# Optimization experiments

Measured on AMD Instinct MI355X. Metric: run time of the kernel, lower is better.

## Reference

```python
import jax, jax.numpy as jnp
import numpy as np

N_SKILLS = 1000
N_PROBLEMS = 20000
EMB = 256
TIME_LOG = 5.0
B, S = 32, 2048


def setup_inputs() -> dict:
    key = jax.random.key(0)
    ks = jax.random.split(key, 10)
    skills = jax.random.randint(ks[0], (B, S), 0, N_SKILLS, dtype=jnp.int64) if jax.config.jax_enable_x64 else jax.random.randint(ks[0], (B, S), 0, N_SKILLS, dtype=jnp.int32)
    problems = jax.random.randint(ks[1], (B, S), 0, N_PROBLEMS, dtype=skills.dtype)
    times = jnp.sort(jax.random.randint(ks[2], (B, S), 0, 10_000_000, dtype=skills.dtype), axis=-1)
    labels = jax.random.randint(ks[3], (B, S), 0, 2, dtype=skills.dtype)
    std = 0.01
    alpha_inter_W = std * jax.random.normal(ks[4], (2 * N_SKILLS, EMB), dtype=jnp.float32)
    alpha_skill_W = std * jax.random.normal(ks[5], (N_SKILLS, EMB), dtype=jnp.float32)
    beta_inter_W = std * jax.random.normal(ks[6], (2 * N_SKILLS, EMB), dtype=jnp.float32)
    beta_skill_W = std * jax.random.normal(ks[7], (N_SKILLS, EMB), dtype=jnp.float32)
    problem_base_W = std * jax.random.normal(ks[8], (N_PROBLEMS, 1), dtype=jnp.float32)
    skill_base_W = std * jax.random.normal(ks[9], (N_SKILLS, 1), dtype=jnp.float32)
    return {
        "skills": skills, "problems": problems, "times": times, "labels": labels,
        "alpha_inter_W": alpha_inter_W, "alpha_skill_W": alpha_skill_W,
        "beta_inter_W": beta_inter_W, "beta_skill_W": beta_skill_W,
        "problem_base_W": problem_base_W, "skill_base_W": skill_base_W,
    }


def reference(skills, problems, times, labels,
              alpha_inter_W, alpha_skill_W, beta_inter_W, beta_skill_W,
              problem_base_W, skill_base_W):
    n_skills = alpha_skill_W.shape[0]
    inters = skills + labels * n_skills  # [B,S]

    alpha_src = alpha_inter_W[inters]      # [B,S,E]
    alpha_tgt = alpha_skill_W[skills]      # [B,S,E]
    alphas = jnp.einsum("bse,bte->bst", alpha_src, alpha_tgt)  # [B,S,S]

    beta_src = beta_inter_W[inters]
    beta_tgt = beta_skill_W[skills]
    betas = jnp.einsum("bse,bte->bst", beta_src, beta_tgt)
    betas = jnp.clip(betas + 1.0, 0.0, 10.0)

    t = times.astype(jnp.float32) / 1000.0
    delta_t = jnp.abs(t[:, :, None] - t[:, None, :])
    delta_t = jnp.log(delta_t + 1e-10) / jnp.log(jnp.float32(TIME_LOG))

    cross = alphas * jnp.exp(-betas * delta_t)  # [B,S,S]

    seq_len = skills.shape[1]
    # original keeps strict upper triangle (source i strictly before target j)
    keep = jnp.triu(jnp.ones((seq_len, seq_len), dtype=cross.dtype), k=1)
    sum_t = jnp.sum(cross * keep[None], axis=-2)  # sum over source dim -> [B,S]

    problem_bias = problem_base_W[problems][..., 0]  # [B,S]
    skill_bias = skill_base_W[skills][..., 0]        # [B,S]
    h = problem_bias + skill_bias + sum_t
    return jax.nn.sigmoid(h)
```

## Files before the change

### kernel.cpp

```cpp
#include <hip/hip_runtime.h>
#include <hip/hip_bf16.h>
#include <stdint.h>

#define NSK   1000
#define EMB   256
#define BB    32
#define SS    2048
#define TILE  128
#define NJT   (SS / TILE)
#define NUNIT (NJT * (NJT + 1) / 2)
#define BK    32
#define NCHUNK (EMB / BK)
#define SCALE_INV (1.0f / 4096.0f)

typedef float f32x16 __attribute__((ext_vector_type(16)));
typedef float f32x4  __attribute__((ext_vector_type(4)));
typedef long  longx2 __attribute__((ext_vector_type(2)));

#define OFF_AI8 0
#define OFF_BI8 (2 * NSK * EMB)
#define OFF_AS8 (4 * NSK * EMB)
#define OFF_BS8 (5 * NSK * EMB)
#define TOT8    (6 * NSK * EMB)

__global__ void cvt_tables(const float* __restrict__ ai, const float* __restrict__ bi,
                           const float* __restrict__ as_, const float* __restrict__ bs,
                           int* __restrict__ ws8, float* __restrict__ acc) {
    int g = blockIdx.x * 256 + threadIdx.x;
    if (g < BB * SS) acc[g] = 0.0f;
    if (g * 4 >= TOT8) return;
    int e = g * 4;
    const float* src; int off;
    if (e < OFF_AS8) { if (e < OFF_BI8) { src = ai;  off = e; }
                       else             { src = bi;  off = e - OFF_BI8; } }
    else             { if (e < OFF_BS8) { src = as_; off = e - OFF_AS8; }
                       else             { src = bs;  off = e - OFF_BS8; } }
    const float4 v = *(const float4*)(src + off);
    int lo = __builtin_amdgcn_cvt_pk_fp8_f32(v.x * 64.0f, v.y * 64.0f, 0, false);
    int wd = __builtin_amdgcn_cvt_pk_fp8_f32(v.z * 64.0f, v.w * 64.0f, lo, true);
    ws8[g] = wd;
}

__device__ __attribute__((noinline)) float dot256(const float* __restrict__ a,
                                                  const float* __restrict__ b) {
    float s = 0.0f;
#pragma unroll 8
    for (int k = 0; k < EMB; ++k) s += a[k] * b[k];
    return s;
}

__global__ __launch_bounds__(256, 2) void hawkes_unit(
    const int* __restrict__ skills, const int* __restrict__ times,
    const int* __restrict__ labels, const unsigned char* __restrict__ tab,
    const float* __restrict__ aiW_f, const float* __restrict__ asW_f,
    const float* __restrict__ biW_f, const float* __restrict__ bsW_f,
    float* __restrict__ acc)
{
    __shared__ __align__(16) char  sbuf[3 * 16384];
    __shared__ __align__(16) float t_i[TILE];
    __shared__ __align__(16) float t_j[TILE];
    __shared__ int   idx_i[TILE];
    __shared__ int   idx_j[TILE];
    __shared__ float colsum[TILE];

    const int u  = blockIdx.x;
    const int b  = u / NUNIT;
    const int p  = u - b * NUNIT;
    int jt = (int)((sqrtf(8.0f * (float)p + 1.0f) - 1.0f) * 0.5f);
    while ((jt + 1) * (jt + 2) / 2 <= p) ++jt;
    while (jt * (jt + 1) / 2 > p) --jt;
    const int it   = p - jt * (jt + 1) / 2;
    const bool diag = (it == jt);
    const int j0 = jt * TILE, i0 = it * TILE;

    const int tid = threadIdx.x;
    const int l   = tid & 63;
    const int w   = tid >> 6;
    const int wi  = w >> 1, wj = w & 1;
    const int lane31 = l & 31;
    const int khalf  = l >> 5;

    if (tid < TILE) {
        int j = j0 + tid;
        idx_j[tid] = skills[b * SS + j];
        t_j[tid]   = (float)times[b * SS + j] / 1000.0f;
        colsum[tid] = 0.0f;
    } else {
        int q = tid - TILE;
        int ii = i0 + q;
        idx_i[q] = skills[b * SS + ii] + labels[b * SS + ii] * NSK;
        t_i[q]   = (float)times[b * SS + ii] / 1000.0f;
    }
    __syncthreads();

    const float tj0 = t_j[wj * 64 + lane31];
    const float tj1 = t_j[wj * 64 + 32 + lane31];

    const unsigned char* my_tab = tab + ((w == 0) ? OFF_AI8 : (w == 1) ? OFF_BI8
                                       : (w == 2) ? OFF_AS8 : OFF_BS8);
    const int* my_idx = (w < 2) ? idx_i : idx_j;
    const unsigned char* rowptr[4];
    int wo[4];
#pragma unroll
    for (int m = 0; m < 4; ++m) {
        int r = m * 32 + (l >> 1);
        rowptr[m] = my_tab + (size_t)my_idx[r] * EMB + (l & 1) * 16;
        wo[m] = w * 4096 + m * 1024 + (l & 1) * 512 + (l >> 1) * 8;
    }

#define LOADC(dst, c)                                                  \
    do { _Pragma("unroll")                                             \
        for (int m = 0; m < 4; ++m)                                    \
            dst[m] = *(const longx2*)(rowptr[m] + (c) * BK);           \
    } while (0)
#define WRITEC(src, buf)                                               \
    do { char* db = sbuf + (buf) * 16384;                              \
        _Pragma("unroll")                                              \
        for (int m = 0; m < 4; ++m) {                                  \
            *(long*)(db + wo[m])       = src[m].x;                     \
            *(long*)(db + wo[m] + 256) = src[m].y;                     \
        }                                                              \
    } while (0)

    f32x16 accA[2][2], accB[2][2];
#pragma unroll
    for (int mi = 0; mi < 2; ++mi)
#pragma unroll
        for (int nj = 0; nj < 2; ++nj) { accA[mi][nj] = 0.0f; accB[mi][nj] = 0.0f; }

    longx2 sregA[4], sregB[4];
    LOADC(sregA, 0);
    WRITEC(sregA, 0);
    LOADC(sregA, 1);

    for (int c = 0; c < NCHUNK; ++c) {
        const int cur = c % 3;
        if (c + 2 < NCHUNK) {
            if (c & 1) LOADC(sregA, c + 2);
            else       LOADC(sregB, c + 2);
        }
        __syncthreads();

        const char* sb = sbuf + cur * 16384;
#pragma unroll
        for (int ks = 0; ks < 2; ++ks) {
            long fa[2], fb[2], ga[2], gb[2];
#pragma unroll
            for (int mi = 0; mi < 2; ++mi) {
                int mb = (wi * 2 + mi) * 1024 + ks * 512 + l * 8;
                fa[mi] = *(const long*)(sb + 0    + mb);
                fb[mi] = *(const long*)(sb + 4096 + mb);
            }
#pragma unroll
            for (int nj = 0; nj < 2; ++nj) {
                int nb = (wj * 2 + nj) * 1024 + ks * 512 + l * 8;
                ga[nj] = *(const long*)(sb + 8192  + nb);
                gb[nj] = *(const long*)(sb + 12288 + nb);
            }
#pragma unroll
            for (int mi = 0; mi < 2; ++mi)
#pragma unroll
                for (int nj = 0; nj < 2; ++nj) {
                    accA[mi][nj] = __builtin_amdgcn_mfma_f32_32x32x16_fp8_fp8(
                        fa[mi], ga[nj], accA[mi][nj], 0, 0, 0);
                    accB[mi][nj] = __builtin_amdgcn_mfma_f32_32x32x16_fp8_fp8(
                        fb[mi], gb[nj], accB[mi][nj], 0, 0, 0);
                }
        }

        if (c + 1 < NCHUNK) {
            if (c & 1) WRITEC(sregB, (c + 1) % 3);
            else       WRITEC(sregA, (c + 1) % 3);
        }
    }

    float csum0 = 0.0f, csum1 = 0.0f;
#pragma unroll
    for (int mi = 0; mi < 2; ++mi) {
        const int rbase = (wi * 2 + mi) * 32 + 4 * khalf;
        f32x4 tiv[4];
#pragma unroll
        for (int q = 0; q < 4; ++q) tiv[q] = *(const f32x4*)(t_i + rbase + 8 * q);
#pragma unroll
        for (int nj = 0; nj < 2; ++nj) {
            const float tjv = (nj == 0) ? tj0 : tj1;
            const int   jl  = wj * 64 + nj * 32 + lane31;
            float s = 0.0f;
#pragma unroll
            for (int r = 0; r < 16; ++r) {
                const int q = r >> 2, e = r & 3;
                const int il = rbase + 8 * q + e;
                if (diag && il >= jl) continue;
                float d = fabsf(tiv[q][e] - tjv);
                float alpha, braw;
                if (d == 0.0f) {
                    alpha = dot256(aiW_f + (size_t)idx_i[il] * EMB,
                                   asW_f + (size_t)idx_j[jl] * EMB) * 4096.0f;
                    braw  = dot256(biW_f + (size_t)idx_i[il] * EMB,
                                   bsW_f + (size_t)idx_j[jl] * EMB) * 4096.0f;
                } else {
                    alpha = accA[mi][nj][r];
                    braw  = accB[mi][nj][r];
                }
                float dl   = __builtin_amdgcn_logf(d + 1e-10f) * 0.6213349345596119f;
                float beta = fminf(fmaxf(braw * SCALE_INV + 1.0f, 0.0f), 10.0f);
                s += alpha * __builtin_amdgcn_exp2f(-beta * dl);
            }
            if (nj == 0) csum0 += s; else csum1 += s;
        }
    }
    csum0 *= SCALE_INV;
    csum1 *= SCALE_INV;

    __syncthreads();
    csum0 += __shfl_xor(csum0, 32);
    csum1 += __shfl_xor(csum1, 32);
    if (l < 32) {
        atomicAdd(&colsum[wj * 64 + lane31], csum0);
        atomicAdd(&colsum[wj * 64 + 32 + lane31], csum1);
    }
    __syncthreads();
    if (tid < TILE)
        atomicAdd(&acc[b * SS + j0 + tid], colsum[tid]);
}

__global__ void hawkes_final(const int* __restrict__ skills, const int* __restrict__ problems,
                             const float* __restrict__ pbW, const float* __restrict__ sbW,
                             float* __restrict__ out) {
    int i = blockIdx.x * 256 + threadIdx.x;
    if (i >= BB * SS) return;
    float h = pbW[problems[i]] + sbW[skills[i]] + out[i];
    out[i] = 1.0f / (1.0f + __builtin_amdgcn_exp2f(-h * 1.4426950408889634f));
}

extern "C" void kernel_launch(void* const* d_in, const int* in_sizes, int n_in,
                              void* d_out, int out_size, void* d_ws, size_t ws_size,
                              hipStream_t stream) {
    const int*   skills   = (const int*)d_in[0];
    const int*   problems = (const int*)d_in[1];
    const int*   times    = (const int*)d_in[2];
    const int*   labels   = (const int*)d_in[3];
    const float* aiW      = (const float*)d_in[4];
    const float* asW      = (const float*)d_in[5];
    const float* biW      = (const float*)d_in[6];
    const float* bsW      = (const float*)d_in[7];
    const float* pbW      = (const float*)d_in[8];
    const float* sbW      = (const float*)d_in[9];
    float* out = (float*)d_out;
    unsigned char* tab = (unsigned char*)d_ws;

    cvt_tables<<<(TOT8 / 4 + 255) / 256, 256, 0, stream>>>(aiW, biW, asW, bsW,
                                                           (int*)tab, out);
    hawkes_unit<<<BB * NUNIT, 256, 0, stream>>>(skills, times, labels, tab,
                                                aiW, asW, biW, bsW, out);
    hawkes_final<<<(BB * SS + 255) / 256, 256, 0, stream>>>(skills, problems, pbW, sbW, out);
}
```

Measured before the change: 190.7 us.

## Fuse three kernels into one persistent cooperative kernel with grid syncs

Merges the table conversion, pairwise tile computation and final sigmoid kernels into a single cooperative kernel. A persistent grid of up to 512 blocks loops over the triangular units, with grid.sync separating the phases. The aim is to remove two kernel launches and their inter-kernel gaps. The cost is grid-wide barriers, a static round-robin assignment of tiles that may balance load worse than the hardware block scheduler, and the overhead of a cooperative launch.

```diff
diff --git a/kernel.cpp b/kernel.cpp
--- a/kernel.cpp
+++ b/kernel.cpp
@@ -1,6 +1,9 @@
 #include <hip/hip_runtime.h>
 #include <hip/hip_bf16.h>
+#include <hip/hip_cooperative_groups.h>
 #include <stdint.h>
+
+namespace cg = cooperative_groups;
 
 #define NSK   1000
 #define EMB   256
@@ -23,24 +26,6 @@
 #define OFF_BS8 (5 * NSK * EMB)
 #define TOT8    (6 * NSK * EMB)
 
-__global__ void cvt_tables(const float* __restrict__ ai, const float* __restrict__ bi,
-                           const float* __restrict__ as_, const float* __restrict__ bs,
-                           int* __restrict__ ws8, float* __restrict__ acc) {
-    int g = blockIdx.x * 256 + threadIdx.x;
-    if (g < BB * SS) acc[g] = 0.0f;
-    if (g * 4 >= TOT8) return;
-    int e = g * 4;
-    const float* src; int off;
-    if (e < OFF_AS8) { if (e < OFF_BI8) { src = ai;  off = e; }
-                       else             { src = bi;  off = e - OFF_BI8; } }
-    else             { if (e < OFF_BS8) { src = as_; off = e - OFF_AS8; }
-                       else             { src = bs;  off = e - OFF_BS8; } }
-    const float4 v = *(const float4*)(src + off);
-    int lo = __builtin_amdgcn_cvt_pk_fp8_f32(v.x * 64.0f, v.y * 64.0f, 0, false);
-    int wd = __builtin_amdgcn_cvt_pk_fp8_f32(v.z * 64.0f, v.w * 64.0f, lo, true);
-    ws8[g] = wd;
-}
-
 __device__ __attribute__((noinline)) float dot256(const float* __restrict__ a,
                                                   const float* __restrict__ b) {
     float s = 0.0f;
@@ -49,21 +34,15 @@
     return s;
 }
 
-__global__ __launch_bounds__(256, 2) void hawkes_unit(
+__device__ __forceinline__ void unit_body(
+    int u,
     const int* __restrict__ skills, const int* __restrict__ times,
     const int* __restrict__ labels, const unsigned char* __restrict__ tab,
     const float* __restrict__ aiW_f, const float* __restrict__ asW_f,
     const float* __restrict__ biW_f, const float* __restrict__ bsW_f,
-    float* __restrict__ acc)
+    float* __restrict__ acc,
+    char* sbuf, float* t_i, float* t_j, int* idx_i, int* idx_j, float* colsum)
 {
-    __shared__ __align__(16) char  sbuf[3 * 16384];
-    __shared__ __align__(16) float t_i[TILE];
-    __shared__ __align__(16) float t_j[TILE];
-    __shared__ int   idx_i[TILE];
-    __shared__ int   idx_j[TILE];
-    __shared__ float colsum[TILE];
-
-    const int u  = blockIdx.x;
     const int b  = u / NUNIT;
     const int p  = u - b * NUNIT;
     int jt = (int)((sqrtf(8.0f * (float)p + 1.0f) - 1.0f) * 0.5f);
@@ -173,6 +152,8 @@
             else       WRITEC(sregA, (c + 1) % 3);
         }
     }
+#undef LOADC
+#undef WRITEC
 
     float csum0 = 0.0f, csum1 = 0.0f;
 #pragma unroll
@@ -224,13 +205,51 @@
         atomicAdd(&acc[b * SS + j0 + tid], colsum[tid]);
 }
 
-__global__ void hawkes_final(const int* __restrict__ skills, const int* __restrict__ problems,
-                             const float* __restrict__ pbW, const float* __restrict__ sbW,
-                             float* __restrict__ out) {
-    int i = blockIdx.x * 256 + threadIdx.x;
-    if (i >= BB * SS) return;
-    float h = pbW[problems[i]] + sbW[skills[i]] + out[i];
-    out[i] = 1.0f / (1.0f + __builtin_amdgcn_exp2f(-h * 1.4426950408889634f));
+__global__ __launch_bounds__(256, 2) void hawkes_all(
+    const int* __restrict__ skills, const int* __restrict__ problems,
+    const int* __restrict__ times,  const int* __restrict__ labels,
+    const float* __restrict__ aiW,  const float* __restrict__ asW,
+    const float* __restrict__ biW,  const float* __restrict__ bsW,
+    const float* __restrict__ pbW,  const float* __restrict__ sbW,
+    unsigned char* __restrict__ tab, float* __restrict__ acc)
+{
+    __shared__ __align__(16) char  sbuf[3 * 16384];
+    __shared__ __align__(16) float t_i[TILE];
+    __shared__ __align__(16) float t_j[TILE];
+    __shared__ int   idx_i[TILE];
+    __shared__ int   idx_j[TILE];
+    __shared__ float colsum[TILE];
+
+    cg::grid_group grid = cg::this_grid();
+    const int nthreads = gridDim.x * 256;
+    const int gtid = blockIdx.x * 256 + threadIdx.x;
+
+    for (int g = gtid; g < TOT8 / 4; g += nthreads) {
+        int e = g * 4;
+        const float* src; int off;
+        if (e < OFF_AS8) { if (e < OFF_BI8) { src = aiW; off = e; }
+                           else             { src = biW; off = e - OFF_BI8; } }
+        else             { if (e < OFF_BS8) { src = asW; off = e - OFF_AS8; }
+                           else             { src = bsW; off = e - OFF_BS8; } }
+        const float4 v = *(const float4*)(src + off);
+        int lo = __builtin_amdgcn_cvt_pk_fp8_f32(v.x * 64.0f, v.y * 64.0f, 0, false);
+        int wd = __builtin_amdgcn_cvt_pk_fp8_f32(v.z * 64.0f, v.w * 64.0f, lo, true);
+        ((int*)tab)[g] = wd;
+    }
+    for (int g = gtid; g < BB * SS; g += nthreads) acc[g] = 0.0f;
+
+    grid.sync();
+
+    for (int u = blockIdx.x; u < BB * NUNIT; u += gridDim.x)
+        unit_body(u, skills, times, labels, tab, aiW, asW, biW, bsW, acc,
+                  sbuf, t_i, t_j, idx_i, idx_j, colsum);
+
+    grid.sync();
+
+    for (int i = gtid; i < BB * SS; i += nthreads) {
+        float h = pbW[problems[i]] + sbW[skills[i]] + acc[i];
+        acc[i] = 1.0f / (1.0f + __builtin_amdgcn_exp2f(-h * 1.4426950408889634f));
+    }
 }
 
 extern "C" void kernel_launch(void* const* d_in, const int* in_sizes, int n_in,
@@ -249,9 +268,15 @@
     float* out = (float*)d_out;
     unsigned char* tab = (unsigned char*)d_ws;
 
-    cvt_tables<<<(TOT8 / 4 + 255) / 256, 256, 0, stream>>>(aiW, biW, asW, bsW,
-                                                           (int*)tab, out);
-    hawkes_unit<<<BB * NUNIT, 256, 0, stream>>>(skills, times, labels, tab,
-                                                aiW, asW, biW, bsW, out);
-    hawkes_final<<<(BB * SS + 255) / 256, 256, 0, stream>>>(skills, problems, pbW, sbW, out);
-}
+    int nb = 0;
+    hipOccupancyMaxActiveBlocksPerMultiprocessor(&nb, (const void*)hawkes_all, 256, 0);
+    if (nb < 1) nb = 1;
+    int grid = nb * 256;
+    if (grid > 512) grid = 512;
+
+    void* args[] = {(void*)&skills, (void*)&problems, (void*)&times, (void*)&labels,
+                    (void*)&aiW, (void*)&asW, (void*)&biW, (void*)&bsW,
+                    (void*)&pbW, (void*)&sbW, (void*)&tab, (void*)&out};
+    hipLaunchCooperativeKernel((const void*)hawkes_all, dim3(grid), dim3(256),
+                               args, 0, stream);
+}
```

Result: slower. 316.0 us (+65.7%).

## Use 128x64 rectangular tiles to cut wasted triangular work

Applied to the files above, without the earlier changes.

Replaces the square 128x128 tile decomposition of the strict upper triangle with 128(i) x 64(j) rectangular tiles, enumerated by a new closed-form mapping over 272 units per batch. Finer j granularity along the diagonal means fewer masked-out pairs get computed, and there are more blocks for load balance. In exchange each block loads fewer j rows and reuses the i-side fragments less, raising per-pair load and sync overhead and halving MFMA work per barrier.

```diff
diff --git a/kernel.cpp b/kernel.cpp
--- a/kernel.cpp
+++ b/kernel.cpp
@@ -6,11 +6,13 @@
 #define EMB   256
 #define BB    32
 #define SS    2048
-#define TILE  128
-#define NJT   (SS / TILE)
-#define NUNIT (NJT * (NJT + 1) / 2)
+#define TI    128
+#define TJ    64
+#define NJT64 (SS / TJ)
+#define NUNITB 272
 #define BK    32
 #define NCHUNK (EMB / BK)
+#define LDSB  12288
 #define SCALE_INV (1.0f / 4096.0f)
 
 typedef float f32x16 __attribute__((ext_vector_type(16)));
@@ -56,22 +58,24 @@
     const float* __restrict__ biW_f, const float* __restrict__ bsW_f,
     float* __restrict__ acc)
 {
-    __shared__ __align__(16) char  sbuf[3 * 16384];
-    __shared__ __align__(16) float t_i[TILE];
-    __shared__ __align__(16) float t_j[TILE];
-    __shared__ int   idx_i[TILE];
-    __shared__ int   idx_j[TILE];
-    __shared__ float colsum[TILE];
+    __shared__ __align__(16) char  sbuf[3 * LDSB];
+    __shared__ __align__(16) float t_i[TI];
+    __shared__ __align__(16) float t_j[TJ];
+    __shared__ int   idx_i[TI];
+    __shared__ int   idx_j[TJ];
+    __shared__ float colsum[TJ];
 
     const int u  = blockIdx.x;
-    const int b  = u / NUNIT;
-    const int p  = u - b * NUNIT;
-    int jt = (int)((sqrtf(8.0f * (float)p + 1.0f) - 1.0f) * 0.5f);
-    while ((jt + 1) * (jt + 2) / 2 <= p) ++jt;
-    while (jt * (jt + 1) / 2 > p) --jt;
-    const int it   = p - jt * (jt + 1) / 2;
-    const bool diag = (it == jt);
-    const int j0 = jt * TILE, i0 = it * TILE;
+    const int b  = u / NUNITB;
+    const int p  = u - b * NUNITB;
+    int m = (int)sqrtf((float)p);
+    while ((m + 1) * (m + 2) <= p) ++m;
+    while (m * (m + 1) > p) --m;
+    int jt, it;
+    if (p >= (m + 1) * (m + 1)) { jt = 2 * m + 1; it = p - (m + 1) * (m + 1); }
+    else                        { jt = 2 * m;     it = p - m * (m + 1); }
+    const int j0 = jt * TJ, i0 = it * TI;
+    const bool partial = (i0 + TI - 1 >= j0);
 
     const int tid = threadIdx.x;
     const int l   = tid & 63;
@@ -80,55 +84,62 @@
     const int lane31 = l & 31;
     const int khalf  = l >> 5;
 
-    if (tid < TILE) {
+    if (tid < TJ) {
         int j = j0 + tid;
         idx_j[tid] = skills[b * SS + j];
         t_j[tid]   = (float)times[b * SS + j] / 1000.0f;
         colsum[tid] = 0.0f;
-    } else {
-        int q = tid - TILE;
+    } else if (tid < TJ + TI) {
+        int q = tid - TJ;
         int ii = i0 + q;
         idx_i[q] = skills[b * SS + ii] + labels[b * SS + ii] * NSK;
         t_i[q]   = (float)times[b * SS + ii] / 1000.0f;
     }
     __syncthreads();
 
-    const float tj0 = t_j[wj * 64 + lane31];
-    const float tj1 = t_j[wj * 64 + 32 + lane31];
-
-    const unsigned char* my_tab = tab + ((w == 0) ? OFF_AI8 : (w == 1) ? OFF_BI8
-                                       : (w == 2) ? OFF_AS8 : OFF_BS8);
-    const int* my_idx = (w < 2) ? idx_i : idx_j;
-    const unsigned char* rowptr[4];
-    int wo[4];
-#pragma unroll
-    for (int m = 0; m < 4; ++m) {
-        int r = m * 32 + (l >> 1);
-        rowptr[m] = my_tab + (size_t)my_idx[r] * EMB + (l & 1) * 16;
-        wo[m] = w * 4096 + m * 1024 + (l & 1) * 512 + (l >> 1) * 8;
+    const float tjv = t_j[wj * 32 + lane31];
+    const int   jl  = wj * 32 + lane31;
+
+    const unsigned char* rowptr[3];
+    int wo[3];
+#pragma unroll
+    for (int s = 0; s < 3; ++s) {
+        int mm = w * 3 + s;
+        int tabbase, ldsbase, row;
+        if (mm < 8) {
+            int mb = mm & 3;
+            tabbase = (mm < 4) ? OFF_AI8 : OFF_BI8;
+            ldsbase = ((mm < 4) ? 0 : 4096) + mb * 1024;
+            row = idx_i[mb * 32 + (l >> 1)];
+        } else {
+            int mb = mm & 1;
+            tabbase = (mm < 10) ? OFF_AS8 : OFF_BS8;
+            ldsbase = ((mm < 10) ? 8192 : 10240) + mb * 1024;
+            row = idx_j[mb * 32 + (l >> 1)];
+        }
+        rowptr[s] = tab + tabbase + (size_t)row * EMB + (l & 1) * 16;
+        wo[s] = ldsbase + (l & 1) * 512 + (l >> 1) * 8;
     }
 
 #define LOADC(dst, c)                                                  \
     do { _Pragma("unroll")                                             \
-        for (int m = 0; m < 4; ++m)                                    \
-            dst[m] = *(const longx2*)(rowptr[m] + (c) * BK);           \
+        for (int s = 0; s < 3; ++s)                                    \
+            dst[s] = *(const longx2*)(rowptr[s] + (c) * BK);           \
     } while (0)
 #define WRITEC(src, buf)                                               \
-    do { char* db = sbuf + (buf) * 16384;                              \
+    do { char* db = sbuf + (buf) * LDSB;                               \
         _Pragma("unroll")                                              \
-        for (int m = 0; m < 4; ++m) {                                  \
-            *(long*)(db + wo[m])       = src[m].x;                     \
-            *(long*)(db + wo[m] + 256) = src[m].y;                     \
+        for (int s = 0; s < 3; ++s) {                                  \
+            *(long*)(db + wo[s])       = src[s].x;                     \
+            *(long*)(db + wo[s] + 256) = src[s].y;                     \
         }                                                              \
     } while (0)
 
-    f32x16 accA[2][2], accB[2][2];
-#pragma unroll
-    for (int mi = 0; mi < 2; ++mi)
-#pragma unroll
-        for (int nj = 0; nj < 2; ++nj) { accA[mi][nj] = 0.0f; accB[mi][nj] = 0.0f; }
-
-    longx2 sregA[4], sregB[4];
+    f32x16 accA[2], accB[2];
+#pragma unroll
+    for (int mi = 0; mi < 2; ++mi) { accA[mi] = 0.0f; accB[mi] = 0.0f; }
+
+    longx2 sregA[3], sregB[3];
     LOADC(sregA, 0);
     WRITEC(sregA, 0);
     LOADC(sregA, 1);
@@ -141,31 +152,28 @@
         }
         __syncthreads();
 
-        const char* sb = sbuf + cur * 16384;
+        const char* sb = sbuf + cur * LDSB;
 #pragma unroll
         for (int ks = 0; ks < 2; ++ks) {
-            long fa[2], fb[2], ga[2], gb[2];
+            long fa[2], fb[2], ga, gb;
 #pragma unroll
             for (int mi = 0; mi < 2; ++mi) {
                 int mb = (wi * 2 + mi) * 1024 + ks * 512 + l * 8;
                 fa[mi] = *(const long*)(sb + 0    + mb);
                 fb[mi] = *(const long*)(sb + 4096 + mb);
             }
-#pragma unroll
-            for (int nj = 0; nj < 2; ++nj) {
-                int nb = (wj * 2 + nj) * 1024 + ks * 512 + l * 8;
-                ga[nj] = *(const long*)(sb + 8192  + nb);
-                gb[nj] = *(const long*)(sb + 12288 + nb);
-            }
-#pragma unroll
-            for (int mi = 0; mi < 2; ++mi)
-#pragma unroll
-                for (int nj = 0; nj < 2; ++nj) {
-                    accA[mi][nj] = __builtin_amdgcn_mfma_f32_32x32x16_fp8_fp8(
-                        fa[mi], ga[nj], accA[mi][nj], 0, 0, 0);
-                    accB[mi][nj] = __builtin_amdgcn_mfma_f32_32x32x16_fp8_fp8(
-                        fb[mi], gb[nj], accB[mi][nj], 0, 0, 0);
-                }
+            {
+                int nb = wj * 1024 + ks * 512 + l * 8;
+                ga = *(const long*)(sb + 8192  + nb);
+                gb = *(const long*)(sb + 10240 + nb);
+            }
+#pragma unroll
+            for (int mi = 0; mi < 2; ++mi) {
+                accA[mi] = __builtin_amdgcn_mfma_f32_32x32x16_fp8_fp8(
+                    fa[mi], ga, accA[mi], 0, 0, 0);
+                accB[mi] = __builtin_amdgcn_mfma_f32_32x32x16_fp8_fp8(
+                    fb[mi], gb, accB[mi], 0, 0, 0);
+            }
         }
 
         if (c + 1 < NCHUNK) {
@@ -174,7 +182,7 @@
         }
     }
 
-    float csum0 = 0.0f, csum1 = 0.0f;
+    float csum = 0.0f;
 #pragma unroll
     for (int mi = 0; mi < 2; ++mi) {
         const int rbase = (wi * 2 + mi) * 32 + 4 * khalf;
@@ -182,45 +190,34 @@
 #pragma unroll
         for (int q = 0; q < 4; ++q) tiv[q] = *(const f32x4*)(t_i + rbase + 8 * q);
 #pragma unroll
-        for (int nj = 0; nj < 2; ++nj) {
-            const float tjv = (nj == 0) ? tj0 : tj1;
-            const int   jl  = wj * 64 + nj * 32 + lane31;
-            float s = 0.0f;
-#pragma unroll
-            for (int r = 0; r < 16; ++r) {
-                const int q = r >> 2, e = r & 3;
-                const int il = rbase + 8 * q + e;
-                if (diag && il >= jl) continue;
-                float d = fabsf(tiv[q][e] - tjv);
-                float alpha, braw;
-                if (d == 0.0f) {
-                    alpha = dot256(aiW_f + (size_t)idx_i[il] * EMB,
-                                   asW_f + (size_t)idx_j[jl] * EMB) * 4096.0f;
-                    braw  = dot256(biW_f + (size_t)idx_i[il] * EMB,
-                                   bsW_f + (size_t)idx_j[jl] * EMB) * 4096.0f;
-                } else {
-                    alpha = accA[mi][nj][r];
-                    braw  = accB[mi][nj][r];
-                }
-                float dl   = __builtin_amdgcn_logf(d + 1e-10f) * 0.6213349345596119f;
-                float beta = fminf(fmaxf(braw * SCALE_INV + 1.0f, 0.0f), 10.0f);
-                s += alpha * __builtin_amdgcn_exp2f(-beta * dl);
-            }
-            if (nj == 0) csum0 += s; else csum1 += s;
-        }
-    }
-    csum0 *= SCALE_INV;
-    csum1 *= SCALE_INV;
+        for (int r = 0; r < 16; ++r) {
+            const int q = r >> 2, e = r & 3;
+            const int il = rbase + 8 * q + e;
+            if (partial && i0 + il >= j0 + jl) continue;
+            float d = fabsf(tiv[q][e] - tjv);
+            float alpha, braw;
+            if (d == 0.0f) {
+                alpha = dot256(aiW_f + (size_t)idx_i[il] * EMB,
+                               asW_f + (size_t)idx_j[jl] * EMB) * 4096.0f;
+                braw  = dot256(biW_f + (size_t)idx_i[il] * EMB,
+                               bsW_f + (size_t)idx_j[jl] * EMB) * 4096.0f;
+            } else {
+                alpha = accA[mi][r];
+                braw  = accB[mi][r];
+            }
+            float dl   = __builtin_amdgcn_logf(d + 1e-10f) * 0.6213349345596119f;
+            float beta = fminf(fmaxf(braw * SCALE_INV + 1.0f, 0.0f), 10.0f);
+            csum += alpha * __builtin_amdgcn_exp2f(-beta * dl);
+        }
+    }
+    csum *= SCALE_INV;
 
     __syncthreads();
-    csum0 += __shfl_xor(csum0, 32);
-    csum1 += __shfl_xor(csum1, 32);
-    if (l < 32) {
-        atomicAdd(&colsum[wj * 64 + lane31], csum0);
-        atomicAdd(&colsum[wj * 64 + 32 + lane31], csum1);
-    }
+    csum += __shfl_xor(csum, 32);
+    if (l < 32)
+        atomicAdd(&colsum[wj * 32 + lane31], csum);
     __syncthreads();
-    if (tid < TILE)
+    if (tid < TJ)
         atomicAdd(&acc[b * SS + j0 + tid], colsum[tid]);
 }
 
@@ -251,7 +248,7 @@
 
     cvt_tables<<<(TOT8 / 4 + 255) / 256, 256, 0, stream>>>(aiW, biW, asW, bsW,
                                                            (int*)tab, out);
-    hawkes_unit<<<BB * NUNIT, 256, 0, stream>>>(skills, times, labels, tab,
-                                                aiW, asW, biW, bsW, out);
+    hawkes_unit<<<BB * NUNITB, 256, 0, stream>>>(skills, times, labels, tab,
+                                                 aiW, asW, biW, bsW, out);
     hawkes_final<<<(BB * SS + 255) / 256, 256, 0, stream>>>(skills, problems, pbW, sbW, out);
 }
```

After: 186.0 us. 2.5% less time.
